# Optimization experiments

Measured on AMD Instinct MI355X. Metric: run time of the kernel, lower is better.

Reference implementation:

```python
import jax, jax.numpy as jnp
import numpy as np
import math

H = 1024  # hidden_size
BELOW = 1024
ABOVE = 1024
B = 2048  # batch


def setup_inputs() -> dict:
    key = jax.random.key(0)
    ks = jax.random.split(key, 10)
    stdv = 1.0 / math.sqrt(H)
    W_hh = jax.random.uniform(ks[0], (4 * H + 1, BELOW), minval=-stdv, maxval=stdv, dtype=jnp.float32)
    U_11 = jax.random.uniform(ks[1], (4 * H + 1, H), minval=-stdv, maxval=stdv, dtype=jnp.float32)
    U_21 = jax.random.uniform(ks[2], (4 * H + 1, ABOVE), minval=-stdv, maxval=stdv, dtype=jnp.float32)
    bias = jax.random.uniform(ks[3], (4 * H + 1,), minval=-stdv, maxval=stdv, dtype=jnp.float32)
    bias = bias.at[-1].set(2.0 / math.sqrt(H))  # reset_parameters sets last bias entry
    c = jax.random.normal(ks[4], (H, B), dtype=jnp.float32)
    h_bottom = jax.random.normal(ks[5], (BELOW, B), dtype=jnp.float32)
    h = jax.random.normal(ks[6], (H, B), dtype=jnp.float32)
    h_top = jax.random.normal(ks[7], (ABOVE, B), dtype=jnp.float32)
    z = jax.random.bernoulli(ks[8], 0.5, (1, B)).astype(jnp.float32)
    z_bottom = jax.random.bernoulli(ks[9], 0.5, (1, B)).astype(jnp.float32)
    return {"c": c, "h_bottom": h_bottom, "h": h, "h_top": h_top, "z": z,
            "z_bottom": z_bottom, "W_hh": W_hh, "U_11": U_11, "U_21": U_21, "bias": bias}


def hard_sigmoid(x, slope=1.0):
    return jnp.clip((x * slope + 1.0) / 2.0, 0.0, 1.0)


def binary_threshold_ste(z_hat, threshold=0.5):
    hard = (z_hat > threshold).astype(z_hat.dtype)
    # straight-through: forward hard, backward identity
    return z_hat + jax.lax.stop_gradient(hard - z_hat)


def reference(c, h_bottom, h, h_top, z, z_bottom, W_hh, U_11, U_21, bias):
    a = 1.0
    s_recur = W_hh @ h_bottom                 # (4H+1, B)
    s_topdown = z * (U_21 @ h_top)            # (4H+1, B)
    s_bottomup = z * (U_11 @ h)               # (4H+1, B)
    f_slice = s_recur + s_topdown + s_bottomup + bias[:, None]
    forgetgate = f_slice[0 * H:1 * H]
    ingate = f_slice[1 * H:2 * H]
    outgate = f_slice[2 * H:3 * H]
    cellgate = f_slice[3 * H:4 * H]
    z_gate = f_slice[4 * H:4 * H + 1]         # (1, B)
    f = jax.nn.sigmoid(forgetgate)
    i = jax.nn.sigmoid(ingate)
    o = jax.nn.sigmoid(outgate)
    g = jnp.tanh(cellgate)
    z_hat = hard_sigmoid(z_gate, slope=a)
    one = 1.0
    c_new = z * (i * g) + (one - z) * (one - z_bottom) * c + (one - z) * z_bottom * (f * c + i * g)
    tanh_c = jnp.tanh(c_new)
    h_new = z * o * tanh_c + (one - z) * (one - z_bottom) * h + (one - z) * z_bottom * o * tanh_c
    z_new = binary_threshold_ste(z_hat)
    return (h_new, c_new, z_new)
```

## Files before the change

kernel.cpp:

```cpp
#include <hip/hip_runtime.h>
#include <hip/hip_bf16.h>

#define HB_ELEMS ((size_t)1024 * 2048)
#define P_ELEMS  ((size_t)4096 * 2048)

typedef __bf16 bfx8 __attribute__((ext_vector_type(8)));
typedef float f32x4 __attribute__((ext_vector_type(4)));

__device__ __forceinline__ float b2f(unsigned short u) {
    union { unsigned int i; float f; } v; v.i = ((unsigned int)u) << 16; return v.f;
}
__device__ __forceinline__ unsigned short f2b(float f) {
    __hip_bfloat16 h = __float2bfloat16(f);
    return *reinterpret_cast<unsigned short*>(&h);
}
__device__ __forceinline__ float loadf(const void* p, size_t i, bool f32) {
    return f32 ? ((const float*)p)[i] : b2f(((const unsigned short*)p)[i]);
}
__device__ __forceinline__ float sigf(float x) { return 1.0f / (1.0f + __expf(-x)); }

__device__ __forceinline__ void cell_math(float fp, float ip, float op, float gp,
                                           float cc, float hh, float zc, float zv,
                                           float& hn, float& cn) {
    float f = sigf(fp), i = sigf(ip), o = sigf(op), g = tanhf(gp);
    float ig = i * g;
    cn = zc * ig + (1.0f - zc) * (1.0f - zv) * cc + (1.0f - zc) * zv * (f * cc + ig);
    float tc = tanhf(cn);
    hn = zc * o * tc + (1.0f - zc) * (1.0f - zv) * hh + (1.0f - zc) * zv * o * tc;
}

__global__ void detect_k(const unsigned short* __restrict__ w, int* __restrict__ flag) {
    int lane = threadIdx.x;
    bool hit = false;
    #pragma unroll
    for (int i = 0; i < 4; ++i) {
        unsigned e = (w[lane + i * 64] >> 7) & 0xFF;
        hit |= (e >= 126);
    }
    unsigned long long m = __ballot(hit);
    if (lane == 0) *flag = (m != 0ULL) ? 1 : 0;
}

__global__ __launch_bounds__(256) void build_bt(
    const void* __restrict__ hb, const void* __restrict__ h,
    const void* __restrict__ ht, const void* __restrict__ z,
    unsigned short* __restrict__ BT, const int* __restrict__ flagp)
{
    const bool f32 = (*flagp != 0);
    int tid = blockIdx.x * 256 + threadIdx.x;
    int b   = tid & 2047;
    int kg8 = tid >> 11;
    int k   = kg8 * 8;

    const void* src; int kl; bool sc;
    if (k < 1024)      { src = hb; kl = k;        sc = false; }
    else if (k < 2048) { src = h;  kl = k - 1024; sc = true;  }
    else               { src = ht; kl = k - 2048; sc = true;  }

    bool zero = sc && (loadf(z, b, f32) == 0.0f);
    unsigned short t[8];
    if (zero) {
        #pragma unroll
        for (int j = 0; j < 8; ++j) t[j] = 0;
    } else if (f32) {
        #pragma unroll
        for (int j = 0; j < 8; ++j) t[j] = f2b(((const float*)src)[(size_t)(kl + j) * 2048 + b]);
    } else {
        #pragma unroll
        for (int j = 0; j < 8; ++j) t[j] = ((const unsigned short*)src)[(size_t)(kl + j) * 2048 + b];
    }
    uint4 v;
    v.x = (unsigned)t[0] | ((unsigned)t[1] << 16);
    v.y = (unsigned)t[2] | ((unsigned)t[3] << 16);
    v.z = (unsigned)t[4] | ((unsigned)t[5] << 16);
    v.w = (unsigned)t[6] | ((unsigned)t[7] << 16);
    *reinterpret_cast<uint4*>(&BT[(size_t)b * 3072 + k]) = v;
}

__global__ __launch_bounds__(256, 2) void gemm_split(
    const void* __restrict__ Whh, const void* __restrict__ U11, const void* __restrict__ U21,
    const unsigned short* __restrict__ BT,
    unsigned short* __restrict__ P, const int* __restrict__ flagp)
{
    const bool f32 = (*flagp != 0);
    __shared__ __align__(16) unsigned short As[2][128 * 64];
    __shared__ __align__(16) unsigned short Bs[2][128 * 64];

    int id  = (blockIdx.z * 32 + blockIdx.y) * 16 + blockIdx.x;
    int sid = (id & 7) * 192 + (id >> 3);
    const int n0   = (sid & 15) * 128;
    const int j0   = ((sid >> 4) & 31) * 32;
    const int kseg = sid >> 9;
    const void* Asrc = (kseg == 0) ? Whh : ((kseg == 1) ? U11 : U21);
    const int kbase = kseg * 1024;

    const int wave = threadIdx.x >> 6;
    const int lane = threadIdx.x & 63;
    const int srow = wave * 8 + (lane >> 3);
    const int scol = (lane & 7) * 8;
    const int lr = lane & 15, kg = lane >> 4;

    f32x4 acc[8][2] = {};

    auto stage = [&](int buf, int k0) {
        #pragma unroll
        for (int r = 0; r < 4; ++r) {
            const unsigned short* g = &BT[(size_t)(n0 + r * 32 + srow) * 3072 + kbase + k0 + scol];
            __builtin_amdgcn_global_load_lds(
                (const __attribute__((address_space(1))) void*)g,
                (__attribute__((address_space(3))) void*)((char*)&Bs[buf][0] + r * 4096 + wave * 1024),
                16, 0, 0);
        }
        if (!f32) {
            #pragma unroll
            for (int r = 0; r < 4; ++r) {
                const unsigned short* g = (const unsigned short*)Asrc
                    + (size_t)(r * 1024 + j0 + srow) * 1024 + k0 + scol;
                __builtin_amdgcn_global_load_lds(
                    (const __attribute__((address_space(1))) void*)g,
                    (__attribute__((address_space(3))) void*)((char*)&As[buf][0] + r * 4096 + wave * 1024),
                    16, 0, 0);
            }
        } else {
            #pragma unroll
            for (int r = 0; r < 4; ++r) {
                int trow = r * 32 + srow;
                const float* g = (const float*)Asrc + (size_t)(r * 1024 + j0 + srow) * 1024 + k0 + scol;
                float4 a0 = *reinterpret_cast<const float4*>(g);
                float4 a1 = *reinterpret_cast<const float4*>(g + 4);
                uint4 v;
                v.x = (unsigned)f2b(a0.x) | ((unsigned)f2b(a0.y) << 16);
                v.y = (unsigned)f2b(a0.z) | ((unsigned)f2b(a0.w) << 16);
                v.z = (unsigned)f2b(a1.x) | ((unsigned)f2b(a1.y) << 16);
                v.w = (unsigned)f2b(a1.z) | ((unsigned)f2b(a1.w) << 16);
                *reinterpret_cast<uint4*>(&As[buf][trow * 64 + scol]) = v;
            }
        }
    };

    stage(0, 0);
    __syncthreads();

    #pragma unroll 2
    for (int t = 0; t < 16; ++t) {
        const int cur = t & 1;
        if (t < 15) stage(cur ^ 1, (t + 1) * 64);

        #pragma unroll
        for (int kk = 0; kk < 64; kk += 32) {
            bfx8 bv0 = *reinterpret_cast<const bfx8*>(&Bs[cur][(wave * 32 + lr) * 64 + kk + kg * 8]);
            bfx8 bv1 = *reinterpret_cast<const bfx8*>(&Bs[cur][(wave * 32 + 16 + lr) * 64 + kk + kg * 8]);
            #pragma unroll
            for (int mi = 0; mi < 8; ++mi) {
                bfx8 af = *reinterpret_cast<const bfx8*>(&As[cur][(mi * 16 + lr) * 64 + kk + kg * 8]);
                acc[mi][0] = __builtin_amdgcn_mfma_f32_16x16x32_bf16(af, bv0, acc[mi][0], 0, 0, 0);
                acc[mi][1] = __builtin_amdgcn_mfma_f32_16x16x32_bf16(af, bv1, acc[mi][1], 0, 0, 0);
            }
        }
        __syncthreads();
    }

    unsigned short* Pp = P + (size_t)kseg * P_ELEMS;
    #pragma unroll
    for (int mi = 0; mi < 8; ++mi) {
        #pragma unroll
        for (int ni = 0; ni < 2; ++ni) {
            int b = n0 + wave * 32 + ni * 16 + lr;
            #pragma unroll
            for (int r = 0; r < 4; ++r) {
                int trow = mi * 16 + kg * 4 + r;
                int gate = trow >> 5, jj = trow & 31;
                size_t m = (size_t)gate * 1024 + j0 + jj;
                Pp[m * 2048 + b] = f2b(acc[mi][ni][r]);
            }
        }
    }
}

__global__ __launch_bounds__(256) void epilogue_split(
    const unsigned short* __restrict__ P, const void* __restrict__ c_,
    const void* __restrict__ h_, const void* __restrict__ z_,
    const void* __restrict__ zb_, const void* __restrict__ bias_,
    void* __restrict__ out_, const int* __restrict__ flagp)
{
    const bool f32 = (*flagp != 0);
    int tid = blockIdx.x * 256 + threadIdx.x;
    int j = tid >> 9;
    int b = (tid & 511) << 2;
    const size_t jb = (size_t)j * 2048 + b;

    float pre[4][4];
    #pragma unroll
    for (int g = 0; g < 4; ++g) {
        size_t row = (size_t)(g * 1024 + j) * 2048 + b;
        ushort4 s0 = *reinterpret_cast<const ushort4*>(&P[row]);
        ushort4 s1 = *reinterpret_cast<const ushort4*>(&P[P_ELEMS + row]);
        ushort4 s2 = *reinterpret_cast<const ushort4*>(&P[2 * P_ELEMS + row]);
        float bv = loadf(bias_, g * 1024 + j, f32);
        pre[g][0] = b2f(s0.x) + b2f(s1.x) + b2f(s2.x) + bv;
        pre[g][1] = b2f(s0.y) + b2f(s1.y) + b2f(s2.y) + bv;
        pre[g][2] = b2f(s0.z) + b2f(s1.z) + b2f(s2.z) + bv;
        pre[g][3] = b2f(s0.w) + b2f(s1.w) + b2f(s2.w) + bv;
    }

    float hn[4], cn[4];
    #pragma unroll
    for (int e = 0; e < 4; ++e) {
        float zc = loadf(z_, b + e, f32);
        float zv = loadf(zb_, b + e, f32);
        float cc = loadf(c_, jb + e, f32);
        float hh = loadf(h_, jb + e, f32);
        cell_math(pre[0][e], pre[1][e], pre[2][e], pre[3][e], cc, hh, zc, zv, hn[e], cn[e]);
    }
    if (f32) {
        float4 ho = {hn[0], hn[1], hn[2], hn[3]};
        float4 co = {cn[0], cn[1], cn[2], cn[3]};
        *reinterpret_cast<float4*>(&((float*)out_)[jb]) = ho;
        *reinterpret_cast<float4*>(&((float*)out_)[HB_ELEMS + jb]) = co;
    } else {
        ushort4 ho = {f2b(hn[0]), f2b(hn[1]), f2b(hn[2]), f2b(hn[3])};
        ushort4 co = {f2b(cn[0]), f2b(cn[1]), f2b(cn[2]), f2b(cn[3])};
        *reinterpret_cast<ushort4*>(&((unsigned short*)out_)[jb]) = ho;
        *reinterpret_cast<ushort4*>(&((unsigned short*)out_)[HB_ELEMS + jb]) = co;
    }
}

__global__ __launch_bounds__(256) void gemm_fused(
    const void* __restrict__ Whh, const void* __restrict__ U11, const void* __restrict__ U21,
    const unsigned short* __restrict__ BT,
    const void* __restrict__ c_, const void* __restrict__ h_,
    const void* __restrict__ z_, const void* __restrict__ zb_,
    const void* __restrict__ bias_, void* __restrict__ out_,
    const int* __restrict__ flagp)
{
    const bool f32 = (*flagp != 0);
    __shared__ __align__(16) unsigned short As[128 * 64];
    __shared__ __align__(16) unsigned short Bs[128 * 64];

    const int n0 = blockIdx.x * 128;
    const int j0 = blockIdx.y * 32;
    const int wave = threadIdx.x >> 6;
    const int lane = threadIdx.x & 63;
    const int srow = wave * 8 + (lane >> 3);
    const int scol = (lane & 7) * 8;
    const int lr = lane & 15, kg = lane >> 4;

    f32x4 acc[8][2] = {};

    for (int k0 = 0; k0 < 3072; k0 += 64) {
        int seg = k0 >> 10, kl = k0 & 1023;
        const void* Asrc = (seg == 0) ? Whh : ((seg == 1) ? U11 : U21);

        __syncthreads();
        #pragma unroll
        for (int r = 0; r < 4; ++r) {
            const unsigned short* g = &BT[(size_t)(n0 + r * 32 + srow) * 3072 + k0 + scol];
            __builtin_amdgcn_global_load_lds(
                (const __attribute__((address_space(1))) void*)g,
                (__attribute__((address_space(3))) void*)((char*)Bs + r * 4096 + wave * 1024),
                16, 0, 0);
        }
        if (!f32) {
            #pragma unroll
            for (int r = 0; r < 4; ++r) {
                const unsigned short* g = (const unsigned short*)Asrc
                    + (size_t)(r * 1024 + j0 + srow) * 1024 + kl + scol;
                __builtin_amdgcn_global_load_lds(
                    (const __attribute__((address_space(1))) void*)g,
                    (__attribute__((address_space(3))) void*)((char*)As + r * 4096 + wave * 1024),
                    16, 0, 0);
            }
        } else {
            #pragma unroll
            for (int r = 0; r < 4; ++r) {
                int trow = r * 32 + srow;
                const float* g = (const float*)Asrc + (size_t)(r * 1024 + j0 + srow) * 1024 + kl + scol;
                float4 a0 = *reinterpret_cast<const float4*>(g);
                float4 a1 = *reinterpret_cast<const float4*>(g + 4);
                uint4 v;
                v.x = (unsigned)f2b(a0.x) | ((unsigned)f2b(a0.y) << 16);
                v.y = (unsigned)f2b(a0.z) | ((unsigned)f2b(a0.w) << 16);
                v.z = (unsigned)f2b(a1.x) | ((unsigned)f2b(a1.y) << 16);
                v.w = (unsigned)f2b(a1.z) | ((unsigned)f2b(a1.w) << 16);
                *reinterpret_cast<uint4*>(&As[trow * 64 + scol]) = v;
            }
        }
        __syncthreads();

        #pragma unroll
        for (int kk = 0; kk < 64; kk += 32) {
            bfx8 bv0 = *reinterpret_cast<const bfx8*>(&Bs[(wave * 32 + lr) * 64 + kk + kg * 8]);
            bfx8 bv1 = *reinterpret_cast<const bfx8*>(&Bs[(wave * 32 + 16 + lr) * 64 + kk + kg * 8]);
            #pragma unroll
            for (int mi = 0; mi < 8; ++mi) {
                bfx8 af = *reinterpret_cast<const bfx8*>(&As[(mi * 16 + lr) * 64 + kk + kg * 8]);
                acc[mi][0] = __builtin_amdgcn_mfma_f32_16x16x32_bf16(af, bv0, acc[mi][0], 0, 0, 0);
                acc[mi][1] = __builtin_amdgcn_mfma_f32_16x16x32_bf16(af, bv1, acc[mi][1], 0, 0, 0);
            }
        }
    }

    #pragma unroll
    for (int ni = 0; ni < 2; ++ni) {
        int b = n0 + wave * 32 + ni * 16 + lr;
        float zc = loadf(z_, b, f32);
        float zv = loadf(zb_, b, f32);
        #pragma unroll
        for (int mh = 0; mh < 2; ++mh) {
            #pragma unroll
            for (int r = 0; r < 4; ++r) {
                int j = j0 + mh * 16 + kg * 4 + r;
                float fp = acc[0 + mh][ni][r] + loadf(bias_, j, f32);
                float ip = acc[2 + mh][ni][r] + loadf(bias_, 1024 + j, f32);
                float op = acc[4 + mh][ni][r] + loadf(bias_, 2048 + j, f32);
                float gp = acc[6 + mh][ni][r] + loadf(bias_, 3072 + j, f32);
                float cc = loadf(c_, (size_t)j * 2048 + b, f32);
                float hh = loadf(h_, (size_t)j * 2048 + b, f32);
                float hn, cn;
                cell_math(fp, ip, op, gp, cc, hh, zc, zv, hn, cn);
                if (f32) {
                    ((float*)out_)[(size_t)j * 2048 + b] = hn;
                    ((float*)out_)[HB_ELEMS + (size_t)j * 2048 + b] = cn;
                } else {
                    ((unsigned short*)out_)[(size_t)j * 2048 + b] = f2b(hn);
                    ((unsigned short*)out_)[HB_ELEMS + (size_t)j * 2048 + b] = f2b(cn);
                }
            }
        }
    }
}

__global__ __launch_bounds__(256) void zrow_part(
    const void* __restrict__ Whh, const void* __restrict__ U11, const void* __restrict__ U21,
    const void* __restrict__ hb, const void* __restrict__ h, const void* __restrict__ ht,
    float* __restrict__ pz, const int* __restrict__ flagp)
{
    const bool f32 = (*flagp != 0);
    const int c   = blockIdx.x;
    const int mat = c >> 5;
    const int k0  = (c & 31) * 32;
    const int b0  = threadIdx.x * 8;

    const void* W = (mat == 0) ? Whh : ((mat == 1) ? U11 : U21);
    const void* X = (mat == 0) ? hb  : ((mat == 1) ? h   : ht);
    const size_t wrow = (size_t)4096 * 1024;

    float acc[8] = {0.f, 0.f, 0.f, 0.f, 0.f, 0.f, 0.f, 0.f};
    if (!f32) {
        const unsigned short* Wp = (const unsigned short*)W;
        const unsigned short* Xp = (const unsigned short*)X;
        #pragma unroll 4
        for (int kk = 0; kk < 32; ++kk) {
            int k = k0 + kk;
            float w = b2f(Wp[wrow + k]);
            ushort4 xa = *reinterpret_cast<const ushort4*>(&Xp[(size_t)k * 2048 + b0]);
            ushort4 xb = *reinterpret_cast<const ushort4*>(&Xp[(size_t)k * 2048 + b0 + 4]);
            acc[0] += w * b2f(xa.x); acc[1] += w * b2f(xa.y);
            acc[2] += w * b2f(xa.z); acc[3] += w * b2f(xa.w);
            acc[4] += w * b2f(xb.x); acc[5] += w * b2f(xb.y);
            acc[6] += w * b2f(xb.z); acc[7] += w * b2f(xb.w);
        }
    } else {
        const float* Wp = (const float*)W;
        const float* Xp = (const float*)X;
        #pragma unroll 4
        for (int kk = 0; kk < 32; ++kk) {
            int k = k0 + kk;
            float w = Wp[wrow + k];
            float4 xa = *reinterpret_cast<const float4*>(&Xp[(size_t)k * 2048 + b0]);
            float4 xb = *reinterpret_cast<const float4*>(&Xp[(size_t)k * 2048 + b0 + 4]);
            acc[0] += w * xa.x; acc[1] += w * xa.y; acc[2] += w * xa.z; acc[3] += w * xa.w;
            acc[4] += w * xb.x; acc[5] += w * xb.y; acc[6] += w * xb.z; acc[7] += w * xb.w;
        }
    }
    #pragma unroll
    for (int j = 0; j < 8; ++j)
        pz[(size_t)c * 2048 + b0 + j] = acc[j];
}

__global__ __launch_bounds__(256) void zrow_reduce(
    const float* __restrict__ pz, const void* __restrict__ z_,
    const void* __restrict__ bias_, void* __restrict__ out_,
    const int* __restrict__ flagp)
{
    const bool f32 = (*flagp != 0);
    int b = blockIdx.x * 256 + threadIdx.x;
    float a1 = 0.f, a2 = 0.f, a3 = 0.f;
    #pragma unroll
    for (int c = 0; c < 32; ++c)  a1 += pz[(size_t)c * 2048 + b];
    #pragma unroll
    for (int c = 32; c < 64; ++c) a2 += pz[(size_t)c * 2048 + b];
    #pragma unroll
    for (int c = 64; c < 96; ++c) a3 += pz[(size_t)c * 2048 + b];
    float zc = loadf(z_, b, f32);
    float s = a1 + zc * (a2 + a3) + loadf(bias_, 4096, f32);
    float zh = (s + 1.0f) * 0.5f;
    zh = fminf(fmaxf(zh, 0.0f), 1.0f);
    float zn = (zh > 0.5f) ? 1.0f : 0.0f;
    if (f32) ((float*)out_)[2 * HB_ELEMS + b] = zn;
    else     ((unsigned short*)out_)[2 * HB_ELEMS + b] = f2b(zn);
}

__global__ __launch_bounds__(256) void zrow_k(
    const void* __restrict__ Whh, const void* __restrict__ U11, const void* __restrict__ U21,
    const void* __restrict__ hb, const void* __restrict__ h, const void* __restrict__ ht,
    const void* __restrict__ z_, const void* __restrict__ bias_,
    void* __restrict__ out_, const int* __restrict__ flagp)
{
    const bool f32 = (*flagp != 0);
    int b = blockIdx.x * 256 + threadIdx.x;
    float a1 = 0.f, a2 = 0.f, a3 = 0.f;
    const size_t wrow = (size_t)4096 * 1024;
    for (int k = 0; k < 1024; ++k) {
        a1 += loadf(Whh, wrow + k, f32) * loadf(hb, (size_t)k * 2048 + b, f32);
        a2 += loadf(U11, wrow + k, f32) * loadf(h,  (size_t)k * 2048 + b, f32);
        a3 += loadf(U21, wrow + k, f32) * loadf(ht, (size_t)k * 2048 + b, f32);
    }
    float zc = loadf(z_, b, f32);
    float s = a1 + zc * (a2 + a3) + loadf(bias_, 4096, f32);
    float zh = (s + 1.0f) * 0.5f;
    zh = fminf(fmaxf(zh, 0.0f), 1.0f);
    float zn = (zh > 0.5f) ? 1.0f : 0.0f;
    if (f32) ((float*)out_)[2 * HB_ELEMS + b] = zn;
    else     ((unsigned short*)out_)[2 * HB_ELEMS + b] = f2b(zn);
}

__global__ __launch_bounds__(256) void fallback_k(
    const void* __restrict__ Whh, const void* __restrict__ U11, const void* __restrict__ U21,
    const void* __restrict__ hb, const void* __restrict__ h, const void* __restrict__ ht,
    const void* __restrict__ c_, const void* __restrict__ z_, const void* __restrict__ zb_,
    const void* __restrict__ bias_, void* __restrict__ out_, const int* __restrict__ flagp)
{
    const bool f32 = (*flagp != 0);
    int b = blockIdx.x * 256 + threadIdx.x;
    int j = blockIdx.y;
    float zc = loadf(z_, b, f32);
    float a[4] = {0.f, 0.f, 0.f, 0.f};
    for (int k = 0; k < 1024; ++k) {
        float xb = loadf(hb, (size_t)k * 2048 + b, f32);
        #pragma unroll
        for (int g = 0; g < 4; ++g)
            a[g] += loadf(Whh, (size_t)(g * 1024 + j) * 1024 + k, f32) * xb;
    }
    for (int k = 0; k < 1024; ++k) {
        float xh = zc * loadf(h, (size_t)k * 2048 + b, f32);
        #pragma unroll
        for (int g = 0; g < 4; ++g)
            a[g] += loadf(U11, (size_t)(g * 1024 + j) * 1024 + k, f32) * xh;
    }
    for (int k = 0; k < 1024; ++k) {
        float xt = zc * loadf(ht, (size_t)k * 2048 + b, f32);
        #pragma unroll
        for (int g = 0; g < 4; ++g)
            a[g] += loadf(U21, (size_t)(g * 1024 + j) * 1024 + k, f32) * xt;
    }
    float fp = a[0] + loadf(bias_, j, f32);
    float ip = a[1] + loadf(bias_, 1024 + j, f32);
    float op = a[2] + loadf(bias_, 2048 + j, f32);
    float gp = a[3] + loadf(bias_, 3072 + j, f32);
    float cc = loadf(c_, (size_t)j * 2048 + b, f32);
    float hh = loadf(h,  (size_t)j * 2048 + b, f32);
    float zv = loadf(zb_, b, f32);
    float hn, cn;
    cell_math(fp, ip, op, gp, cc, hh, zc, zv, hn, cn);
    if (f32) {
        ((float*)out_)[(size_t)j * 2048 + b] = hn;
        ((float*)out_)[HB_ELEMS + (size_t)j * 2048 + b] = cn;
    } else {
        ((unsigned short*)out_)[(size_t)j * 2048 + b] = f2b(hn);
        ((unsigned short*)out_)[HB_ELEMS + (size_t)j * 2048 + b] = f2b(cn);
    }
}

extern "C" void kernel_launch(void* const* d_in, const int* in_sizes, int n_in,
                              void* d_out, int out_size, void* d_ws, size_t ws_size,
                              hipStream_t stream)
{
    const void* c    = d_in[0];
    const void* hb   = d_in[1];
    const void* h    = d_in[2];
    const void* ht   = d_in[3];
    const void* z    = d_in[4];
    const void* zb   = d_in[5];
    const void* Whh  = d_in[6];
    const void* U11  = d_in[7];
    const void* U21  = d_in[8];
    const void* bias = d_in[9];

    int* flag = (int*)d_ws;
    unsigned short* BT = (unsigned short*)((char*)d_ws + 4096);
    const size_t bt_bytes = (size_t)2048 * 3072 * 2;
    float* pz = (float*)((char*)d_ws + 4096 + bt_bytes);
    const size_t pz_bytes = (size_t)96 * 2048 * 4;
    unsigned short* P = (unsigned short*)((char*)d_ws + 4096 + bt_bytes + pz_bytes);
    const size_t p_bytes = 3 * P_ELEMS * 2;

    const size_t need_bt    = 4096 + bt_bytes;
    const size_t need_pz    = need_bt + pz_bytes;
    const size_t need_split = need_pz + p_bytes;

    if (ws_size < 4) return;

    detect_k<<<1, 64, 0, stream>>>((const unsigned short*)Whh, flag);

    if (ws_size >= need_split) {
        build_bt<<<(2048 * 384) / 256, 256, 0, stream>>>(hb, h, ht, z, BT, flag);
        gemm_split<<<dim3(16, 32, 3), 256, 0, stream>>>(Whh, U11, U21, BT, P, flag);
        epilogue_split<<<(1024 * 512) / 256, 256, 0, stream>>>(P, c, h, z, zb, bias, d_out, flag);
    } else if (ws_size >= need_bt) {
        build_bt<<<(2048 * 384) / 256, 256, 0, stream>>>(hb, h, ht, z, BT, flag);
        gemm_fused<<<dim3(16, 32), 256, 0, stream>>>(Whh, U11, U21, BT,
                                                     c, h, z, zb, bias, d_out, flag);
    } else {
        fallback_k<<<dim3(8, 1024), 256, 0, stream>>>(Whh, U11, U21, hb, h, ht,
                                                      c, z, zb, bias, d_out, flag);
    }

    if (ws_size >= need_pz) {
        zrow_part<<<96, 256, 0, stream>>>(Whh, U11, U21, hb, h, ht, pz, flag);
        zrow_reduce<<<8, 256, 0, stream>>>(pz, z, bias, d_out, flag);
    } else {
        zrow_k<<<8, 256, 0, stream>>>(Whh, U11, U21, hb, h, ht, z, bias, d_out, flag);
    }
}
```

Baseline: 151.3 us.

## Use 2x2 wave tiling and XOR-swizzled LDS layout in split GEMM

```diff
diff --git a/kernel.cpp b/kernel.cpp
--- a/kernel.cpp
+++ b/kernel.cpp
@@ -97,15 +97,17 @@
     const int wave = threadIdx.x >> 6;
     const int lane = threadIdx.x & 63;
     const int srow = wave * 8 + (lane >> 3);
-    const int scol = (lane & 7) * 8;
+    const int scol_sw = (((lane & 7) ^ (lane >> 3)) * 8);
+    const int wm = wave >> 1, wn = wave & 1;
     const int lr = lane & 15, kg = lane >> 4;
-
-    f32x4 acc[8][2] = {};
+    const int lr7 = lr & 7;
+
+    f32x4 acc[4][4] = {};
 
     auto stage = [&](int buf, int k0) {
         #pragma unroll
         for (int r = 0; r < 4; ++r) {
-            const unsigned short* g = &BT[(size_t)(n0 + r * 32 + srow) * 3072 + kbase + k0 + scol];
+            const unsigned short* g = &BT[(size_t)(n0 + r * 32 + srow) * 3072 + kbase + k0 + scol_sw];
             __builtin_amdgcn_global_load_lds(
                 (const __attribute__((address_space(1))) void*)g,
                 (__attribute__((address_space(3))) void*)((char*)&Bs[buf][0] + r * 4096 + wave * 1024),
@@ -115,7 +117,7 @@
             #pragma unroll
             for (int r = 0; r < 4; ++r) {
                 const unsigned short* g = (const unsigned short*)Asrc
-                    + (size_t)(r * 1024 + j0 + srow) * 1024 + k0 + scol;
+                    + (size_t)(r * 1024 + j0 + srow) * 1024 + k0 + scol_sw;
                 __builtin_amdgcn_global_load_lds(
                     (const __attribute__((address_space(1))) void*)g,
                     (__attribute__((address_space(3))) void*)((char*)&As[buf][0] + r * 4096 + wave * 1024),
@@ -125,7 +127,9 @@
             #pragma unroll
             for (int r = 0; r < 4; ++r) {
                 int trow = r * 32 + srow;
-                const float* g = (const float*)Asrc + (size_t)(r * 1024 + j0 + srow) * 1024 + k0 + scol;
+                int dst  = trow * 64 + scol_sw;
+                const float* g = (const float*)Asrc + (size_t)(r * 1024 + j0 + srow) * 1024
+                               + k0 + (lane & 7) * 8;
                 float4 a0 = *reinterpret_cast<const float4*>(g);
                 float4 a1 = *reinterpret_cast<const float4*>(g + 4);
                 uint4 v;
@@ -133,7 +137,7 @@
                 v.y = (unsigned)f2b(a0.z) | ((unsigned)f2b(a0.w) << 16);
                 v.z = (unsigned)f2b(a1.x) | ((unsigned)f2b(a1.y) << 16);
                 v.w = (unsigned)f2b(a1.z) | ((unsigned)f2b(a1.w) << 16);
-                *reinterpret_cast<uint4*>(&As[buf][trow * 64 + scol]) = v;
+                *reinterpret_cast<uint4*>(&As[buf][dst]) = v;
             }
         }
     };
@@ -148,30 +152,38 @@
 
         #pragma unroll
         for (int kk = 0; kk < 64; kk += 32) {
-            bfx8 bv0 = *reinterpret_cast<const bfx8*>(&Bs[cur][(wave * 32 + lr) * 64 + kk + kg * 8]);
-            bfx8 bv1 = *reinterpret_cast<const bfx8*>(&Bs[cur][(wave * 32 + 16 + lr) * 64 + kk + kg * 8]);
-            #pragma unroll
-            for (int mi = 0; mi < 8; ++mi) {
-                bfx8 af = *reinterpret_cast<const bfx8*>(&As[cur][(mi * 16 + lr) * 64 + kk + kg * 8]);
-                acc[mi][0] = __builtin_amdgcn_mfma_f32_16x16x32_bf16(af, bv0, acc[mi][0], 0, 0, 0);
-                acc[mi][1] = __builtin_amdgcn_mfma_f32_16x16x32_bf16(af, bv1, acc[mi][1], 0, 0, 0);
-            }
+            const int c0 = kk >> 3;
+            const int csw = ((c0 + kg) ^ lr7) * 8;
+            bfx8 av[4], bv[4];
+            #pragma unroll
+            for (int mi = 0; mi < 4; ++mi)
+                av[mi] = *reinterpret_cast<const bfx8*>(
+                    &As[cur][(wm * 64 + mi * 16 + lr) * 64 + csw]);
+            #pragma unroll
+            for (int ni = 0; ni < 4; ++ni)
+                bv[ni] = *reinterpret_cast<const bfx8*>(
+                    &Bs[cur][(wn * 64 + ni * 16 + lr) * 64 + csw]);
+            #pragma unroll
+            for (int mi = 0; mi < 4; ++mi)
+                #pragma unroll
+                for (int ni = 0; ni < 4; ++ni)
+                    acc[mi][ni] = __builtin_amdgcn_mfma_f32_16x16x32_bf16(av[mi], bv[ni], acc[mi][ni], 0, 0, 0);
         }
         __syncthreads();
     }
 
     unsigned short* Pp = P + (size_t)kseg * P_ELEMS;
     #pragma unroll
-    for (int mi = 0; mi < 8; ++mi) {
-        #pragma unroll
-        for (int ni = 0; ni < 2; ++ni) {
-            int b = n0 + wave * 32 + ni * 16 + lr;
+    for (int mi = 0; mi < 4; ++mi) {
+        #pragma unroll
+        for (int ni = 0; ni < 4; ++ni) {
+            int col = n0 + wn * 64 + ni * 16 + lr;
             #pragma unroll
             for (int r = 0; r < 4; ++r) {
-                int trow = mi * 16 + kg * 4 + r;
+                int trow = wm * 64 + mi * 16 + kg * 4 + r;
                 int gate = trow >> 5, jj = trow & 31;
                 size_t m = (size_t)gate * 1024 + j0 + jj;
-                Pp[m * 2048 + b] = f2b(acc[mi][ni][r]);
+                Pp[m * 2048 + col] = f2b(acc[mi][ni][r]);
             }
         }
     }
```

After: 133.8 us. -11.5%, faster.
